# Kernel optimization log

Measured on AMD Instinct MI355X. Metric: run time of the kernel, lower is better.

## Reference

```python
import jax, jax.numpy as jnp
import numpy as np
from jax.scipy.special import logsumexp

B, T, V, C, H, D, SPW, NC = 16, 256, 10000, 4096, 256, 256, 32, 128


def _res(x, w1, b1, w2, b2):
    # ResLayer: x + relu(lin2(relu(lin1(x))))
    return x + jax.nn.relu(jax.nn.relu(x @ w1 + b1) @ w2 + b2)


def _log_phi(x, proj):
    # Performer-style log random features for the softmax kernel (smp param.)
    return x @ proj - 0.5 * jnp.sum(x * x, -1, keepdims=True)


def _log_matmul_exp(a, b):
    # logits[i,j] = logsumexp_d(a[i,d] + b[j,d]), stable, via a single GEMM
    ma = jnp.max(a, -1, keepdims=True)
    mb = jnp.max(b, -1, keepdims=True)
    return jnp.log(jnp.exp(a - ma) @ jnp.exp(b - mb).T) + ma + mb.T


def setup_inputs() -> dict:
    key = jax.random.key(0)
    ks = jax.random.split(key, 12)
    s = 1.0 / np.sqrt(H)  # xavier-ish scale
    inp = {
        "text": jax.random.randint(ks[0], (B, T), 0, V),
        "start_emb": jax.random.normal(ks[1], (H,), jnp.float32) * s,
        "start_w": jax.random.normal(ks[2], (5, H, H), jnp.float32) * s,
        "start_b": jnp.zeros((5, H), jnp.float32),
        "state_emb": jax.random.normal(ks[3], (C, H), jnp.float32) * s,
        "next_state_emb": jax.random.normal(ks[4], (C, H), jnp.float32) * s,
        "preterminal_emb": jax.random.normal(ks[5], (C, H), jnp.float32) * s,
        "terminal_w": jax.random.normal(ks[6], (4, H, H), jnp.float32) * s,
        "terminal_b": jnp.zeros((4, H), jnp.float32),
        "terminal_emb": jax.random.normal(ks[7], (V, H), jnp.float32) * s,
        "projection": jax.random.normal(ks[8], (H, D), jnp.float32),
    }
    # brown-cluster style assignment: each cluster owns SPW disjoint states
    w2c = jax.random.randint(ks[9], (V,), 0, NC)
    c2s = jnp.arange(NC)[:, None] * SPW + jnp.arange(SPW)[None, :]
    inp["word2state"] = c2s[w2c]  # [V, SPW]
    return inp


def reference(text, word2state, start_emb, start_w, start_b, state_emb,
              next_state_emb, preterminal_emb, terminal_w, terminal_b,
              terminal_emb, projection):
    # --- start distribution (tie_start=True uses next_state_emb) ---
    fx = start_emb @ start_w[0] + start_b[0]
    fx = _res(fx, start_w[1], start_b[1], start_w[2], start_b[2])
    fx = _res(fx, start_w[3], start_b[3], start_w[4], start_b[4])
    lpy = _log_phi(next_state_emb, projection)                      # [C, D]
    start_lp = jax.nn.log_softmax(
        _log_matmul_exp(_log_phi(fx[None], projection), lpy)[0])    # [C]
    # --- transition: kernelized low-rank logits, row log-softmax ---
    trans_lp = jax.nn.log_softmax(
        _log_matmul_exp(_log_phi(state_emb, projection), lpy), -1)  # [C, C]
    # --- emission: terminal_mlp + sparse word2state mask ---
    fp = _res(preterminal_emb, terminal_w[0], terminal_b[0], terminal_w[1], terminal_b[1])
    fp = _res(fp, terminal_w[2], terminal_b[2], terminal_w[3], terminal_b[3])
    emit_logits = _log_matmul_exp(_log_phi(fp, projection),
                                  _log_phi(terminal_emb, projection))  # [C, V]
    rows = word2state.reshape(-1)
    cols = jnp.repeat(jnp.arange(V), SPW)
    mask = jnp.zeros((C, V), bool).at[rows, cols].set(True)
    emit_lp = jax.nn.log_softmax(jnp.where(mask, emit_logits, -1e30), -1)
    # --- log-space forward algorithm over clamped sparse states ---
    clamped = word2state[text]                          # [B, T, SPW]
    emit_bt = emit_lp[clamped, text[:, :, None]]        # [B, T, SPW]
    alpha0 = start_lp[clamped[:, 0]] + emit_bt[:, 0]    # [B, SPW]
    xs = (jnp.swapaxes(clamped[:, :-1], 0, 1),
          jnp.swapaxes(clamped[:, 1:], 0, 1),
          jnp.swapaxes(emit_bt[:, 1:], 0, 1))

    def step(alpha, x):
        cp, cc, em = x                                   # [B,SPW] each / em [B,SPW]
        tr = trans_lp[cp[:, :, None], cc[:, None, :]]    # [B, SPW, SPW]
        return logsumexp(alpha[:, :, None] + tr, axis=1) + em, None

    alpha, _ = jax.lax.scan(step, alpha0, xs)
    return logsumexp(alpha, -1)                          # [B] log evidence
```

## Files before the change

kernel.cpp:

```cpp
#include <hip/hip_runtime.h>

#define B_   16
#define T_   256
#define V_   10000
#define C_   4096
#define H_   256
#define NC_  128
#define CAP_ 224
#define MST  33
#define XST  257
#define HST  264

typedef __bf16 bf16x8 __attribute__((ext_vector_type(8)));
typedef unsigned short u16x8 __attribute__((ext_vector_type(8)));
typedef float  f32x4  __attribute__((ext_vector_type(4)));

__device__ inline unsigned short f2bf(float f){
  unsigned int u = __float_as_uint(f);
  u += 0x7FFFu + ((u >> 16) & 1u);
  return (unsigned short)(u >> 16);
}
__device__ inline float bf2f(unsigned short u){
  return __uint_as_float(((unsigned int)u) << 16);
}
__device__ inline f32x4 mfma16(bf16x8 a, bf16x8 b, f32x4 c){
  return __builtin_amdgcn_mfma_f32_16x16x32_bf16(a, b, c, 0, 0, 0);
}
__device__ inline bf16x8 load_cvt8(const float* p){
  u16x8 u;
  #pragma unroll
  for (int i = 0; i < 8; ++i) u[i] = f2bf(p[i]);
  return __builtin_bit_cast(bf16x8, u);
}
__device__ inline void zero_acc(f32x4 acc[2][4]){
  #pragma unroll
  for (int i = 0; i < 2; ++i)
    #pragma unroll
    for (int jx = 0; jx < 4; ++jx) acc[i][jx] = (f32x4){0.f,0.f,0.f,0.f};
}

__device__ inline void fx_accum(const float* __restrict__ W, const float* xh,
                                int j, float* __restrict__ Anext){
  int t = threadIdx.x;
  float p = 0.f;
  #pragma unroll
  for (int i = 0; i < 8; ++i)
    p = fmaf(xh[i], W[(size_t)(8*j + i)*256 + t], p);
  atomicAdd(&Anext[t], p);
}

__device__ inline void mm_A_gf32(const float* __restrict__ A, size_t lda_row0,
    const unsigned short* __restrict__ Bt, int w, int ln, f32x4 acc[2][4]){
  int m16 = ln & 15, q = ln >> 4, c0 = w*64;
  const float* a0 = A + lda_row0 + (size_t)m16*256 + q*8;
  const float* a1 = a0 + 16*256;
  const unsigned short* bp0 = Bt + (size_t)(c0 + m16)*256 + q*8;
  #pragma unroll
  for (int kt = 0; kt < 8; ++kt){
    bf16x8 af0 = load_cvt8(a0 + kt*32);
    bf16x8 af1 = load_cvt8(a1 + kt*32);
    #pragma unroll
    for (int cj = 0; cj < 4; ++cj){
      bf16x8 bfj = *(const bf16x8*)(bp0 + (size_t)cj*16*256 + kt*32);
      acc[0][cj] = mfma16(af0, bfj, acc[0][cj]);
      acc[1][cj] = mfma16(af1, bfj, acc[1][cj]);
    }
  }
}

__device__ inline void mm_A_ldsbf(const unsigned short* sHb,
    const unsigned short* __restrict__ Bt, int w, int ln, f32x4 acc[2][4]){
  int m16 = ln & 15, q = ln >> 4, c0 = w*64;
  const unsigned short* a0 = sHb + m16*HST + q*8;
  const unsigned short* a1 = sHb + (16 + m16)*HST + q*8;
  const unsigned short* bp0 = Bt + (size_t)(c0 + m16)*256 + q*8;
  #pragma unroll
  for (int kt = 0; kt < 8; ++kt){
    bf16x8 af0 = *(const bf16x8*)(a0 + kt*32);
    bf16x8 af1 = *(const bf16x8*)(a1 + kt*32);
    #pragma unroll
    for (int cj = 0; cj < 4; ++cj){
      bf16x8 bfj = *(const bf16x8*)(bp0 + (size_t)cj*16*256 + kt*32);
      acc[0][cj] = mfma16(af0, bfj, acc[0][cj]);
      acc[1][cj] = mfma16(af1, bfj, acc[1][cj]);
    }
  }
}

__device__ inline void mm_A_ldsf32(const float* sX,
    const unsigned short* __restrict__ Bt, int w, int ln, f32x4 acc[2][4],
    float* lnrm){
  int m16 = ln & 15, q = ln >> 4, c0 = w*64;
  const float* a0 = sX + m16*XST + q*8;
  const float* a1 = sX + (16 + m16)*XST + q*8;
  const unsigned short* bp0 = Bt + (size_t)(c0 + m16)*256 + q*8;
  float ss0 = 0.f, ss1 = 0.f;
  #pragma unroll
  for (int kt = 0; kt < 8; ++kt){
    float av0[8], av1[8];
    #pragma unroll
    for (int i2 = 0; i2 < 8; ++i2){ av0[i2] = a0[kt*32 + i2]; av1[i2] = a1[kt*32 + i2]; }
    u16x8 u0, u1;
    #pragma unroll
    for (int i2 = 0; i2 < 8; ++i2){
      u0[i2] = f2bf(av0[i2]); u1[i2] = f2bf(av1[i2]);
      ss0 = fmaf(av0[i2], av0[i2], ss0);
      ss1 = fmaf(av1[i2], av1[i2], ss1);
    }
    bf16x8 af0 = __builtin_bit_cast(bf16x8, u0);
    bf16x8 af1 = __builtin_bit_cast(bf16x8, u1);
    #pragma unroll
    for (int cj = 0; cj < 4; ++cj){
      bf16x8 bfj = *(const bf16x8*)(bp0 + (size_t)cj*16*256 + kt*32);
      acc[0][cj] = mfma16(af0, bfj, acc[0][cj]);
      acc[1][cj] = mfma16(af1, bfj, acc[1][cj]);
    }
  }
  if (lnrm){
    ss0 += __shfl_xor(ss0, 16); ss0 += __shfl_xor(ss0, 32);
    ss1 += __shfl_xor(ss1, 16); ss1 += __shfl_xor(ss1, 32);
    if (w == 0 && q == 0){ lnrm[m16] = 0.5f*ss0; lnrm[16 + m16] = 0.5f*ss1; }
  }
}

__device__ inline void phi_core(const float* __restrict__ A,
    const unsigned short* __restrict__ Bt, int r0, int M, int w, int ln,
    f32x4 acc[2][4], float* lnrm)
{
  int m16 = ln & 15, q = ln >> 4;
  int c0 = w*64;
  int ra0 = r0 + m16;      if (ra0 > M-1) ra0 = M-1;
  int ra1 = r0 + 16 + m16; if (ra1 > M-1) ra1 = M-1;
  const float* a0 = A + (size_t)ra0*256 + q*8;
  const float* a1 = A + (size_t)ra1*256 + q*8;
  const unsigned short* bp0 = Bt + (size_t)(c0 + m16)*256 + q*8;
  float ss0 = 0.f, ss1 = 0.f;
  #pragma unroll
  for (int kt = 0; kt < 8; ++kt){
    float av0[8], av1[8];
    #pragma unroll
    for (int i2 = 0; i2 < 8; ++i2){ av0[i2] = a0[kt*32 + i2]; av1[i2] = a1[kt*32 + i2]; }
    u16x8 u0, u1;
    #pragma unroll
    for (int i2 = 0; i2 < 8; ++i2){
      u0[i2] = f2bf(av0[i2]); u1[i2] = f2bf(av1[i2]);
      ss0 = fmaf(av0[i2], av0[i2], ss0);
      ss1 = fmaf(av1[i2], av1[i2], ss1);
    }
    bf16x8 af0 = __builtin_bit_cast(bf16x8, u0);
    bf16x8 af1 = __builtin_bit_cast(bf16x8, u1);
    #pragma unroll
    for (int cj = 0; cj < 4; ++cj){
      bf16x8 bfj = *(const bf16x8*)(bp0 + (size_t)cj*16*256 + kt*32);
      acc[0][cj] = mfma16(af0, bfj, acc[0][cj]);
      acc[1][cj] = mfma16(af1, bfj, acc[1][cj]);
    }
  }
  ss0 += __shfl_xor(ss0, 16); ss0 += __shfl_xor(ss0, 32);
  ss1 += __shfl_xor(ss1, 16); ss1 += __shfl_xor(ss1, 32);
  if (w == 0 && q == 0){ lnrm[m16] = 0.5f*ss0; lnrm[16 + m16] = 0.5f*ss1; }
}

__device__ inline void dev_phiB(const float* __restrict__ A,
    const unsigned short* __restrict__ projT, unsigned short* __restrict__ Ebp,
    float* __restrict__ S, int r0, float* lnrm)
{
  int tid = threadIdx.x;
  int w = tid >> 6, ln = tid & 63;
  int m16 = ln & 15, q = ln >> 4;
  f32x4 acc[2][4];
  zero_acc(acc);
  phi_core(A, projT, r0, C_, w, ln, acc, lnrm);
  __syncthreads();
  int c0 = w*64;
  #pragma unroll
  for (int cj = 0; cj < 4; ++cj){
    int col = c0 + cj*16 + m16;
    float cs = 0.f;
    #pragma unroll
    for (int ri = 0; ri < 2; ++ri){
      #pragma unroll
      for (int r = 0; r < 4; ++r){
        int row = ri*16 + q*4 + r;
        float e = __expf(acc[ri][cj][r] - lnrm[row]);
        Ebp[(size_t)(r0 + row)*256 + col] = f2bf(e);
        cs += e;
      }
    }
    cs += __shfl_xor(cs, 16); cs += __shfl_xor(cs, 32);
    if (q == 0) atomicAdd(&S[col], cs);
  }
}

__device__ inline void dev_phiA(const float* __restrict__ A,
    const unsigned short* __restrict__ projT, const float* __restrict__ S,
    unsigned short* __restrict__ Eap, int r0,
    float* lnrm, float* sS, float (*wrow)[32], float (*wden)[32])
{
  int tid = threadIdx.x;
  int w = tid >> 6, ln = tid & 63;
  int m16 = ln & 15, q = ln >> 4;
  sS[tid] = S[tid];
  f32x4 acc[2][4];
  zero_acc(acc);
  phi_core(A, projT, r0, C_, w, ln, acc, lnrm);
  __syncthreads();
  int c0 = w*64;
  #pragma unroll
  for (int ri = 0; ri < 2; ++ri){
    #pragma unroll
    for (int r = 0; r < 4; ++r){
      int row = ri*16 + q*4 + r;
      float mv = -1e30f;
      #pragma unroll
      for (int cj = 0; cj < 4; ++cj){
        acc[ri][cj][r] -= lnrm[row];
        mv = fmaxf(mv, acc[ri][cj][r]);
      }
      #pragma unroll
      for (int d = 1; d < 16; d <<= 1) mv = fmaxf(mv, __shfl_xor(mv, d));
      if (m16 == 0) wrow[w][row] = mv;
    }
  }
  __syncthreads();
  float ev[2][4][4];
  float dsum[2][4];
  #pragma unroll
  for (int ri = 0; ri < 2; ++ri){
    #pragma unroll
    for (int r = 0; r < 4; ++r){
      int row = ri*16 + q*4 + r;
      float m = fmaxf(fmaxf(wrow[0][row], wrow[1][row]), fmaxf(wrow[2][row], wrow[3][row]));
      dsum[ri][r] = 0.f;
      #pragma unroll
      for (int cj = 0; cj < 4; ++cj){
        float scol = sS[c0 + cj*16 + m16];
        float e = __expf(acc[ri][cj][r] - m);
        ev[ri][cj][r] = e;
        dsum[ri][r] = fmaf(e, scol, dsum[ri][r]);
      }
      #pragma unroll
      for (int d = 1; d < 16; d <<= 1) dsum[ri][r] += __shfl_xor(dsum[ri][r], d);
      if (m16 == 0) wden[w][row] = dsum[ri][r];
    }
  }
  __syncthreads();
  #pragma unroll
  for (int ri = 0; ri < 2; ++ri){
    #pragma unroll
    for (int r = 0; r < 4; ++r){
      int row = ri*16 + q*4 + r;
      float den = wden[0][row] + wden[1][row] + wden[2][row] + wden[3][row];
      float inv = 1.0f/den;
      #pragma unroll
      for (int cj = 0; cj < 4; ++cj){
        int col = c0 + cj*16 + m16;
        Eap[(size_t)(r0 + row)*256 + col] = f2bf(ev[ri][cj][r]*inv);
      }
    }
  }
}

__device__ inline void phiE_epilogue(f32x4 acc[2][4], unsigned short* __restrict__ E,
    float* __restrict__ mr, int M, int r0, float* lnrm, float (*wrow)[32])
{
  int tid = threadIdx.x;
  int w = tid >> 6, ln = tid & 63;
  int m16 = ln & 15, q = ln >> 4;
  int c0 = w*64;
  #pragma unroll
  for (int ri = 0; ri < 2; ++ri){
    #pragma unroll
    for (int r = 0; r < 4; ++r){
      int row = ri*16 + q*4 + r;
      float mv = -1e30f;
      #pragma unroll
      for (int cj = 0; cj < 4; ++cj){
        acc[ri][cj][r] -= lnrm[row];
        mv = fmaxf(mv, acc[ri][cj][r]);
      }
      #pragma unroll
      for (int d = 1; d < 16; d <<= 1) mv = fmaxf(mv, __shfl_xor(mv, d));
      if (m16 == 0) wrow[w][row] = mv;
    }
  }
  __syncthreads();
  #pragma unroll
  for (int ri = 0; ri < 2; ++ri){
    #pragma unroll
    for (int r = 0; r < 4; ++r){
      int row = ri*16 + q*4 + r;
      int grow = r0 + row;
      float m = fmaxf(fmaxf(wrow[0][row], wrow[1][row]), fmaxf(wrow[2][row], wrow[3][row]));
      if (grow < M){
        #pragma unroll
        for (int cj = 0; cj < 4; ++cj){
          int col = c0 + cj*16 + m16;
          E[(size_t)grow*256 + col] = f2bf(__expf(acc[ri][cj][r] - m));
        }
        if (w == 0 && m16 == 0) mr[grow] = m;
      }
    }
  }
}

__device__ inline void dev_phiE(const float* __restrict__ A,
    const unsigned short* __restrict__ projT, unsigned short* __restrict__ E,
    float* __restrict__ mr, int M, int r0, float* lnrm, float (*wrow)[32])
{
  int tid = threadIdx.x;
  int w = tid >> 6, ln = tid & 63;
  f32x4 acc[2][4];
  zero_acc(acc);
  phi_core(A, projT, r0, M, w, ln, acc, lnrm);
  __syncthreads();
  phiE_epilogue(acc, E, mr, M, r0, lnrm, wrow);
}

__global__ __launch_bounds__(256) void k_prep(
  const float* __restrict__ proj, const float* __restrict__ tw,
  unsigned short* __restrict__ projT, unsigned short* __restrict__ WT,
  const int* __restrict__ w2s, int* __restrict__ cnt, int* __restrict__ list,
  const float* __restrict__ se, const float* __restrict__ sw,
  float* __restrict__ Afx)
{
  int bx = blockIdx.x, tid = threadIdx.x;
  if (bx < 1280){
    int z = bx >> 8, dcol = bx & 255;
    const float* src = (z == 0) ? proj : (tw + (size_t)(z-1)*65536);
    unsigned short* dst = (z == 0) ? projT : (WT + (size_t)(z-1)*65536);
    dst[dcol*256 + tid] = f2bf(src[tid*256 + dcol]);
    return;
  }
  if (bx < 1320){
    int v = (bx - 1280)*256 + tid;
    if (v < V_){
      int k = w2s[v*32] >> 5;
      int pos = atomicAdd(&cnt[k], 1);
      if (pos < CAP_) list[k*CAP_ + pos] = v;
    }
    return;
  }
  int j = bx - 1320;
  float xh[8];
  #pragma unroll
  for (int i = 0; i < 8; ++i) xh[i] = se[8*j + i];
  fx_accum(sw, xh, j, Afx);
}

__global__ __launch_bounds__(256) void k_stageB(
  const float* __restrict__ pre_emb, const unsigned short* __restrict__ WT,
  const float* __restrict__ term_b,
  const unsigned short* __restrict__ projT,
  unsigned short* __restrict__ Epb, float* __restrict__ mpp,
  const float* __restrict__ next_emb, unsigned short* __restrict__ Ebp,
  float* __restrict__ S,
  const float* __restrict__ term_emb, unsigned short* __restrict__ Etb,
  float* __restrict__ mt,
  const float* __restrict__ sw, const float* __restrict__ sb,
  float* __restrict__ Afx)
{
  __shared__ __align__(16) float sX[32*XST];
  __shared__ __align__(16) unsigned short sHb[32*HST];
  __shared__ float lnrm[32];
  __shared__ float wrow[4][32];
  int bx = blockIdx.x, tid = threadIdx.x;
  int w = tid >> 6, ln = tid & 63;
  int m16 = ln & 15, q = ln >> 4;
  int c0 = w*64;
  if (bx < 128){
    int r0 = bx*32;
    f32x4 acc[2][4];
    zero_acc(acc);
    mm_A_gf32(pre_emb, (size_t)r0*256, WT, w, ln, acc);
    #pragma unroll
    for (int ri = 0; ri < 2; ++ri)
      #pragma unroll
      for (int cj = 0; cj < 4; ++cj)
        #pragma unroll
        for (int r = 0; r < 4; ++r){
          int row = ri*16 + q*4 + r, col = c0 + cj*16 + m16;
          sHb[row*HST + col] = f2bf(fmaxf(acc[ri][cj][r] + term_b[col], 0.f));
        }
    __syncthreads();
    zero_acc(acc);
    mm_A_ldsbf(sHb, WT + 65536, w, ln, acc);
    #pragma unroll
    for (int ri = 0; ri < 2; ++ri)
      #pragma unroll
      for (int cj = 0; cj < 4; ++cj)
        #pragma unroll
        for (int r = 0; r < 4; ++r){
          int row = ri*16 + q*4 + r, col = c0 + cj*16 + m16;
          float v = fmaxf(acc[ri][cj][r] + term_b[256 + col], 0.f);
          sX[row*XST + col] = v + pre_emb[(size_t)(r0 + row)*256 + col];
        }
    __syncthreads();
    zero_acc(acc);
    mm_A_ldsf32(sX, WT + 2*65536, w, ln, acc, nullptr);
    __syncthreads();
    #pragma unroll
    for (int ri = 0; ri < 2; ++ri)
      #pragma unroll
      for (int cj = 0; cj < 4; ++cj)
        #pragma unroll
        for (int r = 0; r < 4; ++r){
          int row = ri*16 + q*4 + r, col = c0 + cj*16 + m16;
          sHb[row*HST + col] = f2bf(fmaxf(acc[ri][cj][r] + term_b[512 + col], 0.f));
        }
    __syncthreads();
    zero_acc(acc);
    mm_A_ldsbf(sHb, WT + 3*65536, w, ln, acc);
    #pragma unroll
    for (int ri = 0; ri < 2; ++ri)
      #pragma unroll
      for (int cj = 0; cj < 4; ++cj)
        #pragma unroll
        for (int r = 0; r < 4; ++r){
          int row = ri*16 + q*4 + r, col = c0 + cj*16 + m16;
          sX[row*XST + col] += fmaxf(acc[ri][cj][r] + term_b[768 + col], 0.f);
        }
    __syncthreads();
    zero_acc(acc);
    mm_A_ldsf32(sX, projT, w, ln, acc, lnrm);
    __syncthreads();
    phiE_epilogue(acc, Epb, mpp, C_, r0, lnrm, wrow);
  } else if (bx < 256){
    dev_phiB(next_emb, projT, Ebp, S, (bx - 128)*32, lnrm);
  } else if (bx < 569){
    dev_phiE(term_emb, projT, Etb, mt, V_, (bx - 256)*32, lnrm, wrow);
  } else {
    int j = bx - 569;
    float xh[8];
    #pragma unroll
    for (int i = 0; i < 8; ++i){ int h = 8*j + i; xh[i] = Afx[h] + sb[h]; }
    fx_accum(sw + 65536, xh, j, Afx + 256);
  }
}

__global__ __launch_bounds__(256) void k_stageC(
  const float* __restrict__ state_emb, const unsigned short* __restrict__ projT,
  const float* __restrict__ S, unsigned short* __restrict__ Eap,
  const unsigned short* __restrict__ Epb, const float* __restrict__ mpp,
  const unsigned short* __restrict__ Etb, const float* __restrict__ mt,
  const int* __restrict__ cnt, const int* __restrict__ list,
  float* __restrict__ emit_col,
  const float* __restrict__ sw, const float* __restrict__ sb,
  float* __restrict__ Afx)
{
  __shared__ float lnrm[32];
  __shared__ float sS[256];
  __shared__ float wrow[4][32];
  __shared__ float wden[4][32];
  __shared__ float mtile[8][32];
  __shared__ float stile[8][32];
  __shared__ float mpl[32];
  __shared__ float denl[32];
  int bx = blockIdx.x, tid = threadIdx.x;
  if (bx < 128){
    dev_phiA(state_emb, projT, S, Eap, bx*32, lnrm, sS, wrow, wden);
    return;
  }
  if (bx >= 256){
    int j = bx - 256;
    float xh[8];
    #pragma unroll
    for (int i = 0; i < 8; ++i){ int h = 8*j + i; xh[i] = fmaxf(Afx[256 + h] + sb[256 + h], 0.f); }
    fx_accum(sw + 2*65536, xh, j, Afx + 512);
    return;
  }
  int k = bx - 128;
  int w = tid >> 6, ln = tid & 63;
  int m16 = ln & 15, q = ln >> 4;
  if (tid < 32) mpl[tid] = mpp[k*32 + tid];
  int n = cnt[k]; if (n > CAP_) n = CAP_;
  int nt = (n + 31) >> 5;
  const int* lp = list + k*CAP_;
  bf16x8 af0[8], af1[8];
  {
    const unsigned short* ap0 = Epb + (size_t)(k*32 + m16)*256 + q*8;
    const unsigned short* ap1 = ap0 + 16*256;
    #pragma unroll
    for (int kt = 0; kt < 8; ++kt){
      af0[kt] = *(const bf16x8*)(ap0 + kt*32);
      af1[kt] = *(const bf16x8*)(ap1 + kt*32);
    }
  }
  float lg[2][2][2][4];
  int   vj[2][2];
  #pragma unroll
  for (int u = 0; u < 2; ++u){
    int t = w + u*4;
    if (t >= nt) continue;
    int j0 = t*32 + m16, j1 = j0 + 16;
    int v0 = lp[(j0 < n) ? j0 : 0];
    int v1 = lp[(j1 < n) ? j1 : 0];
    vj[u][0] = v0; vj[u][1] = v1;
    float mt0 = (j0 < n) ? mt[v0] : 0.f;
    float mt1 = (j1 < n) ? mt[v1] : 0.f;
    const unsigned short* bp0 = Etb + (size_t)v0*256 + q*8;
    const unsigned short* bp1 = Etb + (size_t)v1*256 + q*8;
    f32x4 acc[2][2];
    #pragma unroll
    for (int mi = 0; mi < 2; ++mi)
      #pragma unroll
      for (int ni = 0; ni < 2; ++ni) acc[mi][ni] = (f32x4){0.f,0.f,0.f,0.f};
    #pragma unroll
    for (int kt = 0; kt < 8; ++kt){
      bf16x8 b0 = *(const bf16x8*)(bp0 + kt*32);
      bf16x8 b1 = *(const bf16x8*)(bp1 + kt*32);
      acc[0][0] = mfma16(af0[kt], b0, acc[0][0]);
      acc[0][1] = mfma16(af0[kt], b1, acc[0][1]);
      acc[1][0] = mfma16(af1[kt], b0, acc[1][0]);
      acc[1][1] = mfma16(af1[kt], b1, acc[1][1]);
    }
    #pragma unroll
    for (int mi = 0; mi < 2; ++mi){
      #pragma unroll
      for (int r = 0; r < 4; ++r){
        int row = mi*16 + q*4 + r;
        float l0 = (j0 < n) ? (__logf(acc[mi][0][r]) + mpl[row] + mt0) : -1e30f;
        float l1 = (j1 < n) ? (__logf(acc[mi][1][r]) + mpl[row] + mt1) : -1e30f;
        lg[u][mi][0][r] = l0;
        lg[u][mi][1][r] = l1;
        float mv = fmaxf(l0, l1);
        #pragma unroll
        for (int d = 1; d < 16; d <<= 1) mv = fmaxf(mv, __shfl_xor(mv, d));
        float se = __expf(l0 - mv) + __expf(l1 - mv);
        #pragma unroll
        for (int d = 1; d < 16; d <<= 1) se += __shfl_xor(se, d);
        if (m16 == 0){ mtile[t][row] = mv; stile[t][row] = se; }
      }
    }
  }
  __syncthreads();
  if (tid < 32){
    float gm = -1e30f;
    for (int t = 0; t < nt; ++t) gm = fmaxf(gm, mtile[t][tid]);
    float gs = 0.f;
    for (int t = 0; t < nt; ++t) gs += stile[t][tid]*__expf(mtile[t][tid] - gm);
    denl[tid] = gm + __logf(gs);
  }
  __syncthreads();
  #pragma unroll
  for (int u = 0; u < 2; ++u){
    int t = w + u*4;
    if (t >= nt) continue;
    #pragma unroll
    for (int ni = 0; ni < 2; ++ni){
      int j = t*32 + ni*16 + m16;
      if (j >= n) continue;
      float* outp = emit_col + (size_t)vj[u][ni]*32;
      #pragma unroll
      for (int mi = 0; mi < 2; ++mi)
        #pragma unroll
        for (int r = 0; r < 4; ++r){
          int row = mi*16 + q*4 + r;
          outp[row] = lg[u][mi][ni][r] - denl[row];
        }
    }
  }
}

__device__ inline void prod_acc(const float* __restrict__ L0, const float* __restrict__ L1,
                                f32x4 acc[2][2], int ln)
{
  int m16 = ln & 15, q = ln >> 4;
  bf16x8 af[2], bfv[2];
  #pragma unroll
  for (int mi = 0; mi < 2; ++mi){
    const float* p = L0 + (mi*16 + m16)*MST + q*8;
    u16x8 u;
    #pragma unroll
    for (int jj = 0; jj < 8; ++jj) u[jj] = f2bf(p[jj]);
    af[mi] = __builtin_bit_cast(bf16x8, u);
  }
  #pragma unroll
  for (int ni = 0; ni < 2; ++ni){
    u16x8 u;
    #pragma unroll
    for (int jj = 0; jj < 8; ++jj) u[jj] = f2bf(L1[(q*8 + jj)*MST + ni*16 + m16]);
    bfv[ni] = __builtin_bit_cast(bf16x8, u);
  }
  #pragma unroll
  for (int mi = 0; mi < 2; ++mi)
    #pragma unroll
    for (int ni = 0; ni < 2; ++ni) acc[mi][ni] = mfma16(af[mi], bfv[ni], acc[mi][ni]);
}

__device__ inline void wave_norm_store(f32x4 acc[2][2], float* outp,
                                       float sIn, float* sOut, int ln)
{
  int m16 = ln & 15, q = ln >> 4;
  float mx = 0.f;
  #pragma unroll
  for (int mi = 0; mi < 2; ++mi)
    #pragma unroll
    for (int ni = 0; ni < 2; ++ni)
      #pragma unroll
      for (int r = 0; r < 4; ++r) mx = fmaxf(mx, acc[mi][ni][r]);
  #pragma unroll
  for (int d = 1; d < 64; d <<= 1) mx = fmaxf(mx, __shfl_xor(mx, d));
  float inv = 1.0f/mx;
  #pragma unroll
  for (int mi = 0; mi < 2; ++mi)
    #pragma unroll
    for (int ni = 0; ni < 2; ++ni)
      #pragma unroll
      for (int r = 0; r < 4; ++r)
        outp[(mi*16 + q*4 + r)*MST + ni*16 + m16] = acc[mi][ni][r]*inv;
  if (ln == 0) *sOut = sIn + __logf(mx);
}

__device__ inline void norm_store_g16(f32x4 acc[2][2], unsigned short* outp,
                                      float sIn, float* sOutG, int ln)
{
  int m16 = ln & 15, q = ln >> 4;
  float mx = 0.f;
  #pragma unroll
  for (int mi = 0; mi < 2; ++mi)
    #pragma unroll
    for (int ni = 0; ni < 2; ++ni)
      #pragma unroll
      for (int r = 0; r < 4; ++r) mx = fmaxf(mx, acc[mi][ni][r]);
  #pragma unroll
  for (int d = 1; d < 64; d <<= 1) mx = fmaxf(mx, __shfl_xor(mx, d));
  float inv = 1.0f/mx;
  #pragma unroll
  for (int mi = 0; mi < 2; ++mi)
    #pragma unroll
    for (int ni = 0; ni < 2; ++ni)
      #pragma unroll
      for (int r = 0; r < 4; ++r)
        outp[(mi*16 + q*4 + r)*32 + ni*16 + m16] = f2bf(acc[mi][ni][r]*inv);
  if (ln == 0) *sOutG = sIn + __logf(mx);
}

__device__ inline void prod32(const float* L0, const float* L1, float* outp,
                              float sIn, float* sOut, int ln)
{
  f32x4 acc[2][2];
  #pragma unroll
  for (int mi = 0; mi < 2; ++mi)
    #pragma unroll
    for (int ni = 0; ni < 2; ++ni) acc[mi][ni] = (f32x4){0.f,0.f,0.f,0.f};
  prod_acc(L0, L1, acc, ln);
  wave_norm_store(acc, outp, sIn, sOut, ln);
}

__global__ __launch_bounds__(512) void k_chunk(
  const unsigned short* __restrict__ Eap, const unsigned short* __restrict__ Ebp,
  const float* __restrict__ emit_col, const int* __restrict__ text,
  const int* __restrict__ w2s, unsigned short* __restrict__ Gm, float* __restrict__ Gs,
  const float* __restrict__ sw, const float* __restrict__ sb,
  float* __restrict__ Afx)
{
  __shared__ float bufL[8][32*MST];
  __shared__ float bufN[4][32*MST];
  __shared__ float sL[8], sN[4];
  int bx = blockIdx.x;
  int tid = threadIdx.x;
  if (bx >= 512){
    if (tid < 256){
      int j = bx - 512;
      float xh[8];
      #pragma unroll
      for (int i = 0; i < 8; ++i){
        int h = 8*j + i;
        float x0 = Afx[h] + sb[h];
        xh[i] = x0 + fmaxf(Afx[512 + h] + sb[512 + h], 0.f);
      }
      fx_accum(sw + 3*65536, xh, j, Afx + 768);
    }
    return;
  }
  int b = bx >> 5, ch = bx & 31;
  int w = tid >> 6, ln = tid & 63;
  int m16 = ln & 15, q = ln >> 4;
  {
    int s = ch*8 + w;
    float* outp = bufL[w];
    if (s >= 255){
      for (int i = ln; i < 32*32; i += 64){
        int r = i >> 5, c = i & 31;
        outp[r*MST + c] = (r == c) ? 1.f : 0.f;
      }
      if (ln == 0) sL[w] = 0.f;
    } else {
      int vp = text[b*256 + s], vc = text[b*256 + s + 1];
      int bp = w2s[vp*32], bq = w2s[vc*32];
      const unsigned short* a0 = Eap + (size_t)(bp + m16)*256 + q*8;
      const unsigned short* b0 = Ebp + (size_t)(bq + m16)*256 + q*8;
      f32x4 acc[2][2];
      #pragma unroll
      for (int mi = 0; mi < 2; ++mi)
        #pragma unroll
        for (int ni = 0; ni < 2; ++ni) acc[mi][ni] = (f32x4){0.f,0.f,0.f,0.f};
      #pragma unroll
      for (int kt = 0; kt < 8; ++kt){
        bf16x8 a_0 = *(const bf16x8*)(a0 + kt*32);
        bf16x8 a_1 = *(const bf16x8*)(a0 + 16*256 + kt*32);
        bf16x8 b_0 = *(const bf16x8*)(b0 + kt*32);
        bf16x8 b_1 = *(const bf16x8*)(b0 + 16*256 + kt*32);
        acc[0][0] = mfma16(a_0, b_0, acc[0][0]);
        acc[0][1] = mfma16(a_0, b_1, acc[0][1]);
        acc[1][0] = mfma16(a_1, b_0, acc[1][0]);
        acc[1][1] = mfma16(a_1, b_1, acc[1][1]);
      }
      float e0 = __expf(emit_col[(size_t)vc*32 + m16]);
      float e1 = __expf(emit_col[(size_t)vc*32 + 16 + m16]);
      #pragma unroll
      for (int mi = 0; mi < 2; ++mi)
        #pragma unroll
        for (int r = 0; r < 4; ++r){
          acc[mi][0][r] *= e0;
          acc[mi][1][r] *= e1;
        }
      wave_norm_store(acc, outp, 0.f, &sL[w], ln);
    }
  }
  __syncthreads();
  if (w < 4) prod32(bufL[2*w], bufL[2*w+1], bufN[w], sL[2*w] + sL[2*w+1], &sN[w], ln);
  __syncthreads();
  if (w < 2) prod32(bufN[2*w], bufN[2*w+1], bufL[w], sN[2*w] + sN[2*w+1], &sL[w], ln);
  __syncthreads();
  if (w == 0){
    f32x4 acc[2][2];
    #pragma unroll
    for (int mi = 0; mi < 2; ++mi)
      #pragma unroll
      for (int ni = 0; ni < 2; ++ni) acc[mi][ni] = (f32x4){0.f,0.f,0.f,0.f};
    prod_acc(bufL[0], bufL[1], acc, ln);
    norm_store_g16(acc, Gm + (size_t)bx*1024, sL[0] + sL[1], Gs + bx, ln);
  }
}

__device__ inline void load_mat16(const unsigned short* __restrict__ g,
                                  float* __restrict__ d, int ln){
  #pragma unroll
  for (int p = 0; p < 16; ++p){
    int idx = p*64 + ln;
    int r = idx >> 5, c = idx & 31;
    d[r*MST + c] = bf2f(g[idx]);
  }
}

__global__ __launch_bounds__(512) void k_root(
  const unsigned short* __restrict__ Gm, const float* __restrict__ Gs,
  const float* __restrict__ Afx, const float* __restrict__ sb,
  const float* __restrict__ sw, const float* __restrict__ proj,
  const float* __restrict__ S,
  const unsigned short* __restrict__ Ebp, const float* __restrict__ emit_col,
  const int* __restrict__ text, const int* __restrict__ w2s, float* __restrict__ out)
{
  __shared__ float W[8][3][32*MST];
  __shared__ float sW[8], sT[1];
  __shared__ float eafx[256], sX2[256], sH[256];
  __shared__ float gpart[2][256];
  __shared__ float red[4];
  int b = blockIdx.x;
  int tid = threadIdx.x;
  int w = tid >> 6, ln = tid & 63;
  int t = tid & 255, u = tid >> 8;
  if (tid < 256){
    float x0 = Afx[tid] + sb[tid];
    sX2[tid] = x0 + fmaxf(Afx[512 + tid] + sb[512 + tid], 0.f);
    sH[tid]  = fmaxf(Afx[768 + tid] + sb[768 + tid], 0.f);
  }
  __syncthreads();
  {
    float a = 0.f;
    const float* Wp = sw + 4*65536 + (size_t)(128*u)*256 + t;
    #pragma unroll 8
    for (int h = 0; h < 128; ++h) a = fmaf(sH[128*u + h], Wp[(size_t)h*256], a);
    gpart[u][t] = a;
  }
  __syncthreads();
  if (tid < 256){
    float A4 = gpart[0][t] + gpart[1][t];
    float x4 = sX2[t] + fmaxf(A4 + sb[1024 + t], 0.f);
    sX2[t] = x4;
    float v2 = x4*x4;
    #pragma unroll
    for (int d = 1; d < 64; d <<= 1) v2 += __shfl_xor(v2, d);
    if ((t & 63) == 0) red[t >> 6] = v2;
  }
  __syncthreads();
  float nx = red[0] + red[1] + red[2] + red[3];
  {
    float a = 0.f;
    const float* Pp = proj + (size_t)(128*u)*256 + t;
    #pragma unroll 8
    for (int h = 0; h < 128; ++h) a = fmaf(sX2[128*u + h], Pp[(size_t)h*256], a);
    gpart[u][t] = a;
  }
  __syncthreads();
  float pxv = 0.f;
  if (tid < 256){
    pxv = gpart[0][t] + gpart[1][t] - 0.5f*nx;
    float m2 = pxv;
    #pragma unroll
    for (int d = 1; d < 64; d <<= 1) m2 = fmaxf(m2, __shfl_xor(m2, d));
    if ((t & 63) == 0) red[t >> 6] = m2;
  }
  __syncthreads();
  float m2g = fmaxf(fmaxf(red[0], red[1]), fmaxf(red[2], red[3]));
  if (tid < 256) eafx[t] = __expf(pxv - m2g);
  __syncthreads();
  const unsigned short* G = Gm + ((size_t)(b*32 + w*4))*1024;
  const float* gs = Gs + b*32 + w*4;
  load_mat16(G,        W[w][0], ln);
  load_mat16(G + 1024, W[w][1], ln);
  prod32(W[w][0], W[w][1], W[w][2], gs[0] + gs[1], &sW[w], ln);
  load_mat16(G + 2048, W[w][0], ln);
  prod32(W[w][2], W[w][0], W[w][1], sW[w] + gs[2], &sW[w], ln);
  load_mat16(G + 3072, W[w][0], ln);
  prod32(W[w][1], W[w][0], W[w][2], sW[w] + gs[3], &sW[w], ln);
  __syncthreads();
  if (w == 0){
    float sAcc = sW[0];
    const float* cur = W[0][2];
    int dsel = 0;
    for (int j = 1; j < 8; ++j){
      float* dst = dsel ? W[0][1] : W[0][0];
      prod32(cur, W[j][2], dst, sAcc + sW[j], &sT[0], ln);
      sAcc = sT[0];
      cur = dst;
      dsel ^= 1;
    }
    float part = 0.f;
    for (int d = ln; d < 256; d += 64) part = fmaf(eafx[d], S[d], part);
    #pragma unroll
    for (int d2 = 1; d2 < 64; d2 <<= 1) part += __shfl_xor(part, d2);
    float dfx = part;
    int v0 = text[b*256];
    int k0 = w2s[v0*32];
    int j = ln & 31, h = ln >> 5;
    const unsigned short* er = Ebp + (size_t)(k0 + j)*256;
    float dot = 0.f;
    for (int d = h*128; d < h*128 + 128; ++d)
      dot = fmaf(eafx[d], bf2f(er[d]), dot);
    dot += __shfl_xor(dot, 32);
    float z0 = __logf(dot) + emit_col[(size_t)v0*32 + j];
    float mz = z0;
    #pragma unroll
    for (int d2 = 1; d2 < 32; d2 <<= 1) mz = fmaxf(mz, __shfl_xor(mz, d2));
    float an = __expf(z0 - mz);
    float cs = 0.f;
    for (int i = h*16; i < h*16 + 16; ++i)
      cs = fmaf(__shfl(an, i), cur[i*MST + j], cs);
    cs += __shfl_xor(cs, 32);
    float tot = cs;
    #pragma unroll
    for (int d2 = 1; d2 < 32; d2 <<= 1) tot += __shfl_xor(tot, d2);
    if (ln == 0) out[b] = __logf(tot) + mz + sAcc - __logf(dfx);
  }
}

extern "C" void kernel_launch(void* const* d_in, const int* in_sizes, int n_in,
                              void* d_out, int out_size, void* d_ws, size_t ws_size,
                              hipStream_t stream)
{
  (void)in_sizes; (void)n_in; (void)out_size; (void)ws_size;
  const int*   text      = (const int*)  d_in[0];
  const float* start_emb = (const float*)d_in[1];
  const float* start_w   = (const float*)d_in[2];
  const float* start_b   = (const float*)d_in[3];
  const float* state_emb = (const float*)d_in[4];
  const float* next_emb  = (const float*)d_in[5];
  const float* pre_emb   = (const float*)d_in[6];
  const float* term_w    = (const float*)d_in[7];
  const float* term_b    = (const float*)d_in[8];
  const float* term_emb  = (const float*)d_in[9];
  const float* proj      = (const float*)d_in[10];
  const int*   w2s       = (const int*)  d_in[11];
  float* out = (float*)d_out;

  char* base = (char*)d_ws;
  size_t off = 0;
  auto alloc = [&](size_t bytes)->char*{
    char* p = base + off;
    off += (bytes + 255) & ~(size_t)255;
    return p;
  };
  int*   cnt = (int*)  alloc(128*4);
  float* Afx = (float*)alloc(4*256*4);
  float* S   = (float*)alloc(256*4);
  unsigned short* projT = (unsigned short*)alloc((size_t)65536*2);
  unsigned short* WT    = (unsigned short*)alloc((size_t)4*65536*2);
  unsigned short* Epb = (unsigned short*)alloc((size_t)C_*256*2);
  float* mpp  = (float*)alloc((size_t)C_*4);
  unsigned short* Etb = (unsigned short*)alloc((size_t)V_*256*2);
  float* mt   = (float*)alloc((size_t)V_*4);
  unsigned short* Eap = (unsigned short*)alloc((size_t)C_*256*2);
  unsigned short* Ebp = (unsigned short*)alloc((size_t)C_*256*2);
  int* list = (int*)alloc((size_t)128*CAP_*4);
  float* emit_col = (float*)alloc((size_t)V_*32*4);
  unsigned short* Gm = (unsigned short*)alloc((size_t)512*1024*2);
  float* Gs = (float*)alloc((size_t)512*4);

  (void)hipMemsetAsync(cnt, 0, 512 + 4096 + 1024, stream);

  k_prep<<<1352, 256, 0, stream>>>(proj, term_w, projT, WT, w2s, cnt, list,
                                   start_emb, start_w, Afx);
  k_stageB<<<601, 256, 0, stream>>>(pre_emb, WT, term_b, projT, Epb, mpp,
                                    next_emb, Ebp, S, term_emb, Etb, mt,
                                    start_w, start_b, Afx);
  k_stageC<<<288, 256, 0, stream>>>(state_emb, projT, S, Eap,
                                    Epb, mpp, Etb, mt, cnt, list, emit_col,
                                    start_w, start_b, Afx);
  k_chunk<<<544, 512, 0, stream>>>(Eap, Ebp, emit_col, text, w2s, Gm, Gs,
                                   start_w, start_b, Afx);
  k_root<<<16, 512, 0, stream>>>(Gm, Gs, Afx, start_b, start_w, proj, S,
                                 Ebp, emit_col, text, w2s, out);
}
```

Measured before the change: 202.8 us.

## Move state-embedding phi to stage B and defer denominator normalization to chunk kernel

The phi projection of state_emb no longer runs in stage C, where it waited on the full S column sums. It now runs in stage B as extra blocks that emit row-max-normalized exp features (Eab) with no dependency on S. Stage C only computes the per-row denominators (the dot product of Eab with S) into denInv, and the chunk kernel applies that reciprocal while scaling MFMA outputs. This lightens stage C and spreads the work over more parallel blocks in stage B. The cost is an extra per-row denInv load in the chunk loop, and a bf16 rounding step is now applied before the normalization instead of after it.

```diff
diff --git a/kernel.cpp b/kernel.cpp
--- a/kernel.cpp
+++ b/kernel.cpp
@@ -4,7 +4,6 @@
 #define T_   256
 #define V_   10000
 #define C_   4096
-#define H_   256
 #define NC_  128
 #define CAP_ 224
 #define MST  33
@@ -189,75 +188,6 @@
     }
     cs += __shfl_xor(cs, 16); cs += __shfl_xor(cs, 32);
     if (q == 0) atomicAdd(&S[col], cs);
-  }
-}
-
-__device__ inline void dev_phiA(const float* __restrict__ A,
-    const unsigned short* __restrict__ projT, const float* __restrict__ S,
-    unsigned short* __restrict__ Eap, int r0,
-    float* lnrm, float* sS, float (*wrow)[32], float (*wden)[32])
-{
-  int tid = threadIdx.x;
-  int w = tid >> 6, ln = tid & 63;
-  int m16 = ln & 15, q = ln >> 4;
-  sS[tid] = S[tid];
-  f32x4 acc[2][4];
-  zero_acc(acc);
-  phi_core(A, projT, r0, C_, w, ln, acc, lnrm);
-  __syncthreads();
-  int c0 = w*64;
-  #pragma unroll
-  for (int ri = 0; ri < 2; ++ri){
-    #pragma unroll
-    for (int r = 0; r < 4; ++r){
-      int row = ri*16 + q*4 + r;
-      float mv = -1e30f;
-      #pragma unroll
-      for (int cj = 0; cj < 4; ++cj){
-        acc[ri][cj][r] -= lnrm[row];
-        mv = fmaxf(mv, acc[ri][cj][r]);
-      }
-      #pragma unroll
-      for (int d = 1; d < 16; d <<= 1) mv = fmaxf(mv, __shfl_xor(mv, d));
-      if (m16 == 0) wrow[w][row] = mv;
-    }
-  }
-  __syncthreads();
-  float ev[2][4][4];
-  float dsum[2][4];
-  #pragma unroll
-  for (int ri = 0; ri < 2; ++ri){
-    #pragma unroll
-    for (int r = 0; r < 4; ++r){
-      int row = ri*16 + q*4 + r;
-      float m = fmaxf(fmaxf(wrow[0][row], wrow[1][row]), fmaxf(wrow[2][row], wrow[3][row]));
-      dsum[ri][r] = 0.f;
-      #pragma unroll
-      for (int cj = 0; cj < 4; ++cj){
-        float scol = sS[c0 + cj*16 + m16];
-        float e = __expf(acc[ri][cj][r] - m);
-        ev[ri][cj][r] = e;
-        dsum[ri][r] = fmaf(e, scol, dsum[ri][r]);
-      }
-      #pragma unroll
-      for (int d = 1; d < 16; d <<= 1) dsum[ri][r] += __shfl_xor(dsum[ri][r], d);
-      if (m16 == 0) wden[w][row] = dsum[ri][r];
-    }
-  }
-  __syncthreads();
-  #pragma unroll
-  for (int ri = 0; ri < 2; ++ri){
-    #pragma unroll
-    for (int r = 0; r < 4; ++r){
-      int row = ri*16 + q*4 + r;
-      float den = wden[0][row] + wden[1][row] + wden[2][row] + wden[3][row];
-      float inv = 1.0f/den;
-      #pragma unroll
-      for (int cj = 0; cj < 4; ++cj){
-        int col = c0 + cj*16 + m16;
-        Eap[(size_t)(r0 + row)*256 + col] = f2bf(ev[ri][cj][r]*inv);
-      }
-    }
   }
 }
 
@@ -358,7 +288,9 @@
   const float* __restrict__ term_emb, unsigned short* __restrict__ Etb,
   float* __restrict__ mt,
   const float* __restrict__ sw, const float* __restrict__ sb,
-  float* __restrict__ Afx)
+  float* __restrict__ Afx,
+  const float* __restrict__ state_emb, unsigned short* __restrict__ Eab,
+  float* __restrict__ maS)
 {
   __shared__ __align__(16) float sX[32*XST];
   __shared__ __align__(16) unsigned short sHb[32*HST];
@@ -429,47 +361,55 @@
     dev_phiB(next_emb, projT, Ebp, S, (bx - 128)*32, lnrm);
   } else if (bx < 569){
     dev_phiE(term_emb, projT, Etb, mt, V_, (bx - 256)*32, lnrm, wrow);
-  } else {
+  } else if (bx < 601){
     int j = bx - 569;
     float xh[8];
     #pragma unroll
     for (int i = 0; i < 8; ++i){ int h = 8*j + i; xh[i] = Afx[h] + sb[h]; }
     fx_accum(sw + 65536, xh, j, Afx + 256);
+  } else {
+    dev_phiE(state_emb, projT, Eab, maS, C_, (bx - 601)*32, lnrm, wrow);
   }
 }
 
 __global__ __launch_bounds__(256) void k_stageC(
-  const float* __restrict__ state_emb, const unsigned short* __restrict__ projT,
-  const float* __restrict__ S, unsigned short* __restrict__ Eap,
   const unsigned short* __restrict__ Epb, const float* __restrict__ mpp,
   const unsigned short* __restrict__ Etb, const float* __restrict__ mt,
   const int* __restrict__ cnt, const int* __restrict__ list,
   float* __restrict__ emit_col,
+  const unsigned short* __restrict__ Eab, const float* __restrict__ S,
+  float* __restrict__ denInv,
   const float* __restrict__ sw, const float* __restrict__ sb,
   float* __restrict__ Afx)
 {
-  __shared__ float lnrm[32];
-  __shared__ float sS[256];
-  __shared__ float wrow[4][32];
-  __shared__ float wden[4][32];
   __shared__ float mtile[8][32];
   __shared__ float stile[8][32];
   __shared__ float mpl[32];
   __shared__ float denl[32];
   int bx = blockIdx.x, tid = threadIdx.x;
-  if (bx < 128){
-    dev_phiA(state_emb, projT, S, Eap, bx*32, lnrm, sS, wrow, wden);
-    return;
-  }
-  if (bx >= 256){
-    int j = bx - 256;
+  if (bx >= 192){
+    int j = bx - 192;
     float xh[8];
     #pragma unroll
     for (int i = 0; i < 8; ++i){ int h = 8*j + i; xh[i] = fmaxf(Afx[256 + h] + sb[256 + h], 0.f); }
     fx_accum(sw + 2*65536, xh, j, Afx + 512);
     return;
   }
-  int k = bx - 128;
+  if (bx >= 128){
+    int g = bx - 128;
+    int r = g*64 + (tid >> 2);
+    int seg = tid & 3;
+    const unsigned short* er = Eab + (size_t)r*256 + seg*64;
+    const float* sp = S + seg*64;
+    float s = 0.f;
+    #pragma unroll 8
+    for (int i = 0; i < 64; ++i) s = fmaf(bf2f(er[i]), sp[i], s);
+    s += __shfl_xor(s, 1);
+    s += __shfl_xor(s, 2);
+    if (seg == 0) denInv[r] = 1.0f / s;
+    return;
+  }
+  int k = bx;
   int w = tid >> 6, ln = tid & 63;
   int m16 = ln & 15, q = ln >> 4;
   if (tid < 32) mpl[tid] = mpp[k*32 + tid];
@@ -486,6 +426,7 @@
       af1[kt] = *(const bf16x8*)(ap1 + kt*32);
     }
   }
+  __syncthreads();
   float lg[2][2][2][4];
   int   vj[2][2];
   #pragma unroll
@@ -649,9 +590,10 @@
 }
 
 __global__ __launch_bounds__(512) void k_chunk(
-  const unsigned short* __restrict__ Eap, const unsigned short* __restrict__ Ebp,
-  const float* __restrict__ emit_col, const int* __restrict__ text,
-  const int* __restrict__ w2s, unsigned short* __restrict__ Gm, float* __restrict__ Gs,
+  const unsigned short* __restrict__ Eab, const unsigned short* __restrict__ Ebp,
+  const float* __restrict__ emit_col, const float* __restrict__ denInv,
+  const int* __restrict__ text, const int* __restrict__ w2s,
+  unsigned short* __restrict__ Gm, float* __restrict__ Gs,
   const float* __restrict__ sw, const float* __restrict__ sb,
   float* __restrict__ Afx)
 {
@@ -689,7 +631,7 @@
     } else {
       int vp = text[b*256 + s], vc = text[b*256 + s + 1];
       int bp = w2s[vp*32], bq = w2s[vc*32];
-      const unsigned short* a0 = Eap + (size_t)(bp + m16)*256 + q*8;
+      const unsigned short* a0 = Eab + (size_t)(bp + m16)*256 + q*8;
       const unsigned short* b0 = Ebp + (size_t)(bq + m16)*256 + q*8;
       f32x4 acc[2][2];
       #pragma unroll
@@ -713,8 +655,9 @@
       for (int mi = 0; mi < 2; ++mi)
         #pragma unroll
         for (int r = 0; r < 4; ++r){
-          acc[mi][0][r] *= e0;
-          acc[mi][1][r] *= e1;
+          float dn = denInv[bp + mi*16 + q*4 + r];
+          acc[mi][0][r] *= e0*dn;
+          acc[mi][1][r] *= e1*dn;
         }
       wave_norm_store(acc, outp, 0.f, &sL[w], ln);
     }
@@ -892,8 +835,10 @@
   float* mpp  = (float*)alloc((size_t)C_*4);
   unsigned short* Etb = (unsigned short*)alloc((size_t)V_*256*2);
   float* mt   = (float*)alloc((size_t)V_*4);
-  unsigned short* Eap = (unsigned short*)alloc((size_t)C_*256*2);
+  unsigned short* Eab = (unsigned short*)alloc((size_t)C_*256*2);
   unsigned short* Ebp = (unsigned short*)alloc((size_t)C_*256*2);
+  float* maS  = (float*)alloc((size_t)C_*4);
+  float* denInv = (float*)alloc((size_t)C_*4);
   int* list = (int*)alloc((size_t)128*CAP_*4);
   float* emit_col = (float*)alloc((size_t)V_*32*4);
   unsigned short* Gm = (unsigned short*)alloc((size_t)512*1024*2);
@@ -903,14 +848,14 @@
 
   k_prep<<<1352, 256, 0, stream>>>(proj, term_w, projT, WT, w2s, cnt, list,
                                    start_emb, start_w, Afx);
-  k_stageB<<<601, 256, 0, stream>>>(pre_emb, WT, term_b, projT, Epb, mpp,
+  k_stageB<<<729, 256, 0, stream>>>(pre_emb, WT, term_b, projT, Epb, mpp,
                                     next_emb, Ebp, S, term_emb, Etb, mt,
-                                    start_w, start_b, Afx);
-  k_stageC<<<288, 256, 0, stream>>>(state_emb, projT, S, Eap,
-                                    Epb, mpp, Etb, mt, cnt, list, emit_col,
-                                    start_w, start_b, Afx);
-  k_chunk<<<544, 512, 0, stream>>>(Eap, Ebp, emit_col, text, w2s, Gm, Gs,
-                                   start_w, start_b, Afx);
+                                    start_w, start_b, Afx,
+                                    state_emb, Eab, maS);
+  k_stageC<<<224, 256, 0, stream>>>(Epb, mpp, Etb, mt, cnt, list, emit_col,
+                                    Eab, S, denInv, start_w, start_b, Afx);
+  k_chunk<<<544, 512, 0, stream>>>(Eab, Ebp, emit_col, denInv, text, w2s,
+                                   Gm, Gs, start_w, start_b, Afx);
   k_root<<<16, 512, 0, stream>>>(Gm, Gs, Afx, start_b, start_w, proj, S,
                                  Ebp, emit_col, text, w2s, out);
 }
```

After: 198.9 us. About the same (-1.9%).
